# Kernel tuning notes

Measured on AMD Instinct MI355X. Metric: run time of the kernel, lower is better.

The kernel has to match this reference:

```python
import jax, jax.numpy as jnp
import numpy as np


def _lsa_numpy(cost):
    """O(n^3) Jonker-Volgenant / Hungarian (shortest augmenting path with
    potentials). Returns col[i] = column assigned to row i. Matches
    scipy.optimize.linear_sum_assignment for square cost matrices."""
    n = cost.shape[0]
    u = np.zeros(n + 1)
    v = np.zeros(n + 1)
    p = np.zeros(n + 1, dtype=np.int64)   # p[j] = row matched to column j (1-based)
    way = np.zeros(n + 1, dtype=np.int64)
    for i in range(1, n + 1):
        p[0] = i
        j0 = 0
        minv = np.full(n + 1, np.inf)
        used = np.zeros(n + 1, dtype=bool)
        while True:
            used[j0] = True
            i0 = p[j0]
            free = ~used
            free[0] = False
            cur = cost[i0 - 1] - u[i0] - v[1:]
            better = free[1:] & (cur < minv[1:])
            minv[1:] = np.where(better, cur, minv[1:])
            way[1:] = np.where(better, j0, way[1:])
            masked = np.where(free[1:], minv[1:], np.inf)
            j1 = int(np.argmin(masked)) + 1
            delta = masked[j1 - 1]
            u[p[used]] += delta
            v[used] -= delta
            minv[1:] = np.where(free[1:], minv[1:] - delta, minv[1:])
            j0 = j1
            if p[j0] == 0:
                break
        while j0 != 0:
            j1 = int(way[j0])
            p[j0] = p[j1]
            j0 = j1
    col = np.zeros(n, dtype=np.int64)
    for j in range(1, n + 1):
        col[p[j] - 1] = j - 1
    return col


def _batched_lsa(costs):
    costs = np.asarray(costs, dtype=np.float64)
    return np.stack([_lsa_numpy(c) for c in costs]).astype(np.int32)


def _pairwise_dist(pred, target):
    # (B,L,1,D) - (B,1,L,D) -> L2 norm over D, matching torch.norm(x-y, dim=-1)
    return jnp.linalg.norm(pred[:, :, None, :] - target[:, None, :, :], axis=-1)


def setup_inputs() -> dict:
    key = jax.random.key(0)
    k1, k2 = jax.random.split(key)
    B, L, D = 16, 256, 128
    pred = jax.random.normal(k1, (B, L, D), dtype=jnp.float32)
    target = jax.random.normal(k2, (B, L, D), dtype=jnp.float32)
    return {"pred": pred, "target": target}


def reference(pred, target):
    B, L, _ = pred.shape
    dist = _pairwise_dist(pred, target)  # (B, L, L)
    # Hungarian assignment on the detached cost matrices (host callback, like
    # the original's .detach().cpu().numpy() + scipy linear_sum_assignment).
    cols = jax.pure_callback(
        _batched_lsa,
        jax.ShapeDtypeStruct((B, L), jnp.int32),
        jax.lax.stop_gradient(dist),
    )
    # dist[b, r, cols[b, r]] for all rows; reduction='mean' per batch, summed
    # then divided by B == global mean over all matched pairs.
    matched = jnp.take_along_axis(dist, cols[:, :, None], axis=2)[..., 0]  # (B, L)
    return jnp.mean(matched)
```

## Files before the change

### kernel.cpp

```cpp
#include <hip/hip_runtime.h>
#include <hip/hip_fp16.h>
#include <hip/hip_bf16.h>
#include <float.h>
#include <limits.h>

#define B_SZ 16
#define L_SZ 256
#define D_SZ 128

__global__ __launch_bounds__(256) void dist_kernel(const float* __restrict__ pred,
                                                   const float* __restrict__ target,
                                                   float* __restrict__ dist) {
    __shared__ float predRows[8][D_SZ];
    const int blk = blockIdx.x;
    const int b   = blk >> 5;
    const int i0  = (blk & 31) * 8;
    const int tid = threadIdx.x;

    for (int idx = tid; idx < 8 * D_SZ; idx += 256) {
        int r = idx >> 7, d = idx & (D_SZ - 1);
        predRows[r][d] = pred[((size_t)b * L_SZ + i0 + r) * D_SZ + d];
    }
    __syncthreads();

    const int j = tid;
    const float* tr = target + ((size_t)b * L_SZ + j) * D_SZ;
    float acc[8];
#pragma unroll
    for (int r = 0; r < 8; ++r) acc[r] = 0.0f;

    for (int d = 0; d < D_SZ; d += 4) {
        float4 tv = *(const float4*)(tr + d);
#pragma unroll
        for (int r = 0; r < 8; ++r) {
            float4 pv = *(const float4*)(&predRows[r][d]);
            float dx = pv.x - tv.x; acc[r] += dx * dx;
            float dy = pv.y - tv.y; acc[r] += dy * dy;
            float dz = pv.z - tv.z; acc[r] += dz * dz;
            float dw = pv.w - tv.w; acc[r] += dw * dw;
        }
    }
#pragma unroll
    for (int r = 0; r < 8; ++r)
        dist[((size_t)b * L_SZ + i0 + r) * L_SZ + j] = sqrtf(acc[r]);
}

__device__ inline int readlane_i(int x, int l) { return __builtin_amdgcn_readlane(x, l); }
__device__ inline float readlane_f(float x, int l) {
    return __uint_as_float((unsigned)__builtin_amdgcn_readlane((int)__float_as_uint(x), l));
}
__device__ inline unsigned uminu(unsigned a, unsigned b) { return a < b ? a : b; }
template <int CTRL>
__device__ inline unsigned dpp_mov(unsigned v) {
    return (unsigned)__builtin_amdgcn_update_dpp((int)v, (int)v, CTRL, 0xF, 0xF, false);
}
__device__ inline unsigned wave_umin_bcast(unsigned v) {
    unsigned a = dpp_mov<0x111>(v);
    unsigned b = dpp_mov<0x112>(v);
    v = uminu(uminu(v, a), b);
    a = dpp_mov<0x113>(v);
    b = dpp_mov<0x116>(v);
    v = uminu(uminu(v, a), b);
    a = dpp_mov<0x119>(v);
    v = uminu(v, a);
    a = dpp_mov<0x142>(v);
    v = uminu(v, a);
    a = dpp_mov<0x143>(v);
    v = uminu(v, a);
    return (unsigned)__builtin_amdgcn_readlane((int)v, 63);
}
__device__ inline void unpack4(uint2 pk, float& a, float& b, float& c, float& d) {
    union { unsigned u; __half2 h; } x, y; x.u = pk.x; y.u = pk.y;
    a = __low2float(x.h); b = __high2float(x.h);
    c = __low2float(y.h); d = __high2float(y.h);
}
#define SEL4(a0,a1,a2,a3,k) ((k)==0?(a0):(k)==1?(a1):(k)==2?(a2):(a3))

#define OFF_U      (L_SZ * L_SZ * 2)
#define OFF_CLAIM  (OFF_U + (L_SZ + 1) * 4)
#define OFF_FL     (OFF_CLAIM + (L_SZ + 1) * 4)
#define LSA_LDS_BYTES (OFF_FL + (L_SZ + 1) * 4 + 4)

__global__ __launch_bounds__(64) void lsa_kernel(const float* __restrict__ dist,
                                                 double* __restrict__ partial) {
    extern __shared__ char smem[];
    float* u_lds   = (float*)(smem + OFF_U);
    int*   claimed = (int*)(smem + OFF_CLAIM);
    int*   fl      = (int*)(smem + OFF_FL);

    const int b = blockIdx.x;
    const int t = threadIdx.x;
    const float* cost = dist + (size_t)b * L_SZ * L_SZ;
    const int c0i = 4 * t, c1i = 4 * t + 1, c2i = 4 * t + 2, c3i = 4 * t + 3;

    for (int idx = t * 4; idx < L_SZ * L_SZ; idx += 256) {
        float4 f = *(const float4*)(cost + idx);
        union { unsigned u; __half2 h; } a, c;
        a.h = __floats2half2_rn(f.x, f.y);
        c.h = __floats2half2_rn(f.z, f.w);
        uint2 pk; pk.x = a.u; pk.y = c.u;
        *(uint2*)(smem + idx * 2) = pk;
    }
    __syncthreads();

    float bv0 = FLT_MAX, bv1 = FLT_MAX, bv2 = FLT_MAX, bv3 = FLT_MAX;
    int   br0 = 0, br1 = 0, br2 = 0, br3 = 0;
    for (int i = 1; i <= L_SZ; ++i) {
        uint2 cpk = *(const uint2*)(smem + (size_t)(i - 1) * (L_SZ * 2) + t * 8);
        float c0, c1, c2, c3; unpack4(cpk, c0, c1, c2, c3);
        if (c0 < bv0) { bv0 = c0; br0 = i; }
        if (c1 < bv1) { bv1 = c1; br1 = i; }
        if (c2 < bv2) { bv2 = c2; br2 = i; }
        if (c3 < bv3) { bv3 = c3; br3 = i; }
    }
    float v0 = bv0, v1 = bv1, v2 = bv2, v3 = bv3;

    for (int r = t; r <= L_SZ; r += 64) claimed[r] = INT_MAX;
    __syncthreads();
    atomicMin(&claimed[br0], c0i);
    atomicMin(&claimed[br1], c1i);
    atomicMin(&claimed[br2], c2i);
    atomicMin(&claimed[br3], c3i);
    __syncthreads();
    int p0 = (claimed[br0] == c0i) ? br0 : 0;
    int p1 = (claimed[br1] == c1i) ? br1 : 0;
    int p2 = (claimed[br2] == c2i) ? br2 : 0;
    int p3 = (claimed[br3] == c3i) ? br3 : 0;

    int nf = 0;
    for (int blk = 0; blk < 4; ++blk) {
        int r = blk * 64 + t + 1;
        bool isfree = (claimed[r] == INT_MAX);
        unsigned long long mask = __ballot(isfree);
        int before = __popcll(mask & ((1ULL << t) - 1ULL));
        if (isfree) fl[nf + before] = r;
        nf += (int)__popcll(mask);
    }
    __syncthreads();

    int numfree = nf;
    int budget = 1024;
    for (int pass = 0; pass < 2; ++pass) {
        int kq = 0, prv = numfree; numfree = 0;
        while (kq < prv && budget > 0) {
            budget--;
            int i = fl[kq]; kq++;
            uint2 cpk = *(const uint2*)(smem + (size_t)(i - 1) * (L_SZ * 2) + t * 8);
            float cc0, cc1, cc2, cc3; unpack4(cpk, cc0, cc1, cc2, cc3);
            float rc0 = cc0 - v0, rc1 = cc1 - v1, rc2 = cc2 - v2, rc3 = cc3 - v3;
            float m1 = rc0; int j1 = c0i; float m2 = FLT_MAX; int j2 = INT_MAX;
            if (rc1 < m1) { m2 = m1; j2 = j1; m1 = rc1; j1 = c1i; } else if (rc1 < m2) { m2 = rc1; j2 = c1i; }
            if (rc2 < m1) { m2 = m1; j2 = j1; m1 = rc2; j1 = c2i; } else if (rc2 < m2) { m2 = rc2; j2 = c2i; }
            if (rc3 < m1) { m2 = m1; j2 = j1; m1 = rc3; j1 = c3i; } else if (rc3 < m2) { m2 = rc3; j2 = c3i; }
#pragma unroll
            for (int off = 1; off < 64; off <<= 1) {
                float bm1 = __shfl_xor(m1, off, 64); int bj1 = __shfl_xor(j1, off, 64);
                float bm2 = __shfl_xor(m2, off, 64); int bj2 = __shfl_xor(j2, off, 64);
                bool bw = (bm1 < m1) || (bm1 == m1 && bj1 < j1);
                if (bw) {
                    if (bm2 < m1 || (bm2 == m1 && bj2 < j1)) { m2 = bm2; j2 = bj2; }
                    else { m2 = m1; j2 = j1; }
                    m1 = bm1; j1 = bj1;
                } else {
                    if (bm1 < m2 || (bm1 == m2 && bj1 < j2)) { m2 = bm1; j2 = bj1; }
                }
            }
            int t1 = j1 >> 2, k1 = j1 & 3;
            int i0 = readlane_i(SEL4(p0, p1, p2, p3, k1), t1);
            bool strict = (m1 < m2);
            int jt, i0t;
            if (strict) {
                jt = j1; i0t = i0;
                float amt = m2 - m1;
                if (t == t1) {
                    if (k1 == 0) v0 -= amt; else if (k1 == 1) v1 -= amt;
                    else if (k1 == 2) v2 -= amt; else v3 -= amt;
                }
            } else if (i0 != 0) {
                jt = j2; i0t = readlane_i(SEL4(p0, p1, p2, p3, j2 & 3), j2 >> 2);
            } else { jt = j1; i0t = 0; }
            {
                int tt = jt >> 2, kk = jt & 3;
                if (t == tt) {
                    if (kk == 0) p0 = i; else if (kk == 1) p1 = i;
                    else if (kk == 2) p2 = i; else p3 = i;
                }
            }
            if (i0t != 0) {
                if (strict) { kq--; if (t == 0) fl[kq] = i0t; }
                else        { if (t == 0) fl[numfree] = i0t; numfree++; }
            }
            __syncthreads();
        }
        if (budget <= 0) break;
    }

    __syncthreads();
    for (int r = t; r <= L_SZ; r += 64) { claimed[r] = 0; u_lds[r] = 0.0f; }
    __syncthreads();
    if (p0) claimed[p0] = 1;
    if (p1) claimed[p1] = 1;
    if (p2) claimed[p2] = 1;
    if (p3) claimed[p3] = 1;
    __syncthreads();
    int nfree = 0;
    for (int blk = 0; blk < 4; ++blk) {
        int r = blk * 64 + t + 1;
        bool isfree = (claimed[r] == 0);
        unsigned long long mask = __ballot(isfree);
        int before = __popcll(mask & ((1ULL << t) - 1ULL));
        if (isfree) fl[nfree + before] = r;
        nfree += (int)__popcll(mask);
    }
    __syncthreads();
    float pu0 = 0.f, pu1 = 0.f, pu2 = 0.f, pu3 = 0.f;
    const __half* ch = (const __half*)smem;
    if (p0) { pu0 = __half2float(ch[(size_t)(p0 - 1) * L_SZ + c0i]) - v0; u_lds[p0] = pu0; }
    if (p1) { pu1 = __half2float(ch[(size_t)(p1 - 1) * L_SZ + c1i]) - v1; u_lds[p1] = pu1; }
    if (p2) { pu2 = __half2float(ch[(size_t)(p2 - 1) * L_SZ + c2i]) - v2; u_lds[p2] = pu2; }
    if (p3) { pu3 = __half2float(ch[(size_t)(p3 - 1) * L_SZ + c3i]) - v3; u_lds[p3] = pu3; }
    __syncthreads();

    const unsigned HB  = __float_as_uint(1e30f) & 0xFFFFFF00u;
    const unsigned hp0 = HB | (unsigned)c0i, hp1 = HB | (unsigned)c1i;
    const unsigned hp2 = HB | (unsigned)c2i, hp3 = HB | (unsigned)c3i;
    float vsh0 = v0, vsh1 = v1, vsh2 = v2, vsh3 = v3;

    for (int f = 0; f < nfree; ++f) {
        const int icur = fl[f];
        unsigned s0 = 0x7F7FFF00u | (unsigned)c0i;
        unsigned s1 = 0x7F7FFF00u | (unsigned)c1i;
        unsigned s2 = 0x7F7FFF00u | (unsigned)c2i;
        unsigned s3 = 0x7F7FFF00u | (unsigned)c3i;
        int w0 = -1, w1 = -1, w2 = -1, w3 = -1;
        float ds0 = 0.f, ds1 = 0.f, ds2 = 0.f, ds3 = 0.f;
        int   irow = icur;
        float ui0 = u_lds[icur];
        float dj0 = 0.f;
        int   j0  = -1;
        int jS = 0; float dfin = 0.f;

        for (int it = 0; it <= L_SZ; ++it) {
            uint2 cpk = *(const uint2*)(smem + (size_t)(irow - 1) * (L_SZ * 2) + t * 8);
            float cc0, cc1, cc2, cc3; unpack4(cpk, cc0, cc1, cc2, cc3);
            const float base = dj0 - ui0;
            float n0 = fmaxf((cc0 - vsh0) + base, 0.0f);
            float n1 = fmaxf((cc1 - vsh1) + base, 0.0f);
            float n2 = fmaxf((cc2 - vsh2) + base, 0.0f);
            float n3 = fmaxf((cc3 - vsh3) + base, 0.0f);
            unsigned np0 = (__float_as_uint(n0) & 0xFFFFFF00u) | (unsigned)c0i;
            unsigned np1 = (__float_as_uint(n1) & 0xFFFFFF00u) | (unsigned)c1i;
            unsigned np2 = (__float_as_uint(n2) & 0xFFFFFF00u) | (unsigned)c2i;
            unsigned np3 = (__float_as_uint(n3) & 0xFFFFFF00u) | (unsigned)c3i;
            bool b0 = np0 < s0, b1 = np1 < s1, b2 = np2 < s2, b3 = np3 < s3;
            w0 = b0 ? j0 : w0;  s0 = b0 ? np0 : s0;
            w1 = b1 ? j0 : w1;  s1 = b1 ? np1 : s1;
            w2 = b2 ? j0 : w2;  s2 = b2 ? np2 : s2;
            w3 = b3 ? j0 : w3;  s3 = b3 ? np3 : s3;

            unsigned m01 = uminu(s0, s1), m23 = uminu(s2, s3);
            unsigned m4  = uminu(m01, m23);
            int kloc = (int)(m4 & 3u);
            int   myi = SEL4(p0, p1, p2, p3, kloc);
            float myu = SEL4(pu0, pu1, pu2, pu3, kloc);

            const unsigned pk = wave_umin_bcast(m4);
            const int   j1    = (int)(pk & 255u);
            const int   t1    = j1 >> 2;
            const float delta = __uint_as_float(pk & 0xFFFFFF00u);
            const int   i1    = readlane_i(myi, t1);
            const float u1    = readlane_f(myu, t1);

            if (i1 == 0 || it == L_SZ) { jS = j1; dfin = delta; break; }

            bool e0 = (c0i == j1), e1 = (c1i == j1), e2 = (c2i == j1), e3 = (c3i == j1);
            vsh0 = e0 ? -1e30f : vsh0;  s0 = e0 ? hp0 : s0;  ds0 = e0 ? delta : ds0;
            vsh1 = e1 ? -1e30f : vsh1;  s1 = e1 ? hp1 : s1;  ds1 = e1 ? delta : ds1;
            vsh2 = e2 ? -1e30f : vsh2;  s2 = e2 ? hp2 : s2;  ds2 = e2 ? delta : ds2;
            vsh3 = e3 ? -1e30f : vsh3;  s3 = e3 ? hp3 : s3;  ds3 = e3 ? delta : ds3;

            j0 = j1; dj0 = delta; ui0 = u1; irow = i1;
        }

        if (vsh0 < -1e29f) { u_lds[p0] += dfin - ds0; v0 += ds0 - dfin; }
        if (vsh1 < -1e29f) { u_lds[p1] += dfin - ds1; v1 += ds1 - dfin; }
        if (vsh2 < -1e29f) { u_lds[p2] += dfin - ds2; v2 += ds2 - dfin; }
        if (vsh3 < -1e29f) { u_lds[p3] += dfin - ds3; v3 += ds3 - dfin; }
        if (t == 0) u_lds[icur] += dfin;
        vsh0 = v0; vsh1 = v1; vsh2 = v2; vsh3 = v3;
        __syncthreads();

        int j = jS;
        for (int st = 0; st <= L_SZ; ++st) {
            int tj = j >> 2, kj = j & 3;
            int jn = readlane_i(SEL4(w0, w1, w2, w3, kj), tj);
            int pn;
            if (jn < 0) pn = icur;
            else pn = readlane_i(SEL4(p0, p1, p2, p3, jn & 3), jn >> 2);
            if (t == tj) {
                if (kj == 0) p0 = pn; else if (kj == 1) p1 = pn;
                else if (kj == 2) p2 = pn; else p3 = pn;
            }
            if (jn < 0) break;
            j = jn;
        }
        __syncthreads();
        pu0 = u_lds[p0]; pu1 = u_lds[p1]; pu2 = u_lds[p2]; pu3 = u_lds[p3];
        __syncthreads();
    }

    double s = 0.0;
    s += (double)cost[(size_t)max(p0 - 1, 0) * L_SZ + c0i];
    s += (double)cost[(size_t)max(p1 - 1, 0) * L_SZ + c1i];
    s += (double)cost[(size_t)max(p2 - 1, 0) * L_SZ + c2i];
    s += (double)cost[(size_t)max(p3 - 1, 0) * L_SZ + c3i];
#pragma unroll
    for (int off = 1; off < 64; off <<= 1) s += __shfl_xor(s, off, 64);
    if (t == 0) partial[b] = s;
}

__global__ void finalize_kernel(const double* __restrict__ partial, float* __restrict__ out) {
    double s = 0.0;
    for (int b = 0; b < B_SZ; ++b) s += partial[b];
    out[0] = (float)(s / (double)(B_SZ * L_SZ));
}

extern "C" void kernel_launch(void* const* d_in, const int* in_sizes, int n_in,
                              void* d_out, int out_size, void* d_ws, size_t ws_size,
                              hipStream_t stream) {
    const float* pred   = (const float*)d_in[0];
    const float* target = (const float*)d_in[1];
    float* out = (float*)d_out;

    float*  dist    = (float*)d_ws;
    double* partial = (double*)((char*)d_ws + (size_t)B_SZ * L_SZ * L_SZ * sizeof(float));

    (void)hipFuncSetAttribute((const void*)lsa_kernel,
                              hipFuncAttributeMaxDynamicSharedMemorySize,
                              LSA_LDS_BYTES);

    dist_kernel<<<B_SZ * L_SZ / 8, 256, 0, stream>>>(pred, target, dist);
    lsa_kernel<<<B_SZ, 64, LSA_LDS_BYTES, stream>>>(dist, partial);
    finalize_kernel<<<1, 1, 0, stream>>>(partial, out);
}
```

Before: 2.170 ms.

## Speculatively prefetch next Dijkstra row using second-smallest slack candidate

In the Hungarian shortest-augmenting-path inner loop, each lane now keeps both its minimum and second-minimum packed slack. A second wave-wide min reduction predicts the next column to be selected, and that row's cost data is loaded from LDS ahead of time. When the prediction matches the actual next column, the dependent LDS load drops off the serial critical path. The cost is an extra DPP reduction, readlane and LDS load on every iteration, and the prediction can be stale because newly scanned rows lower slacks.

Measured after the change: 2.382 ms. 1.1x slower.

```diff
diff --git a/kernel.cpp b/kernel.cpp
--- a/kernel.cpp
+++ b/kernel.cpp
@@ -50,6 +50,7 @@
     return __uint_as_float((unsigned)__builtin_amdgcn_readlane((int)__float_as_uint(x), l));
 }
 __device__ inline unsigned uminu(unsigned a, unsigned b) { return a < b ? a : b; }
+__device__ inline unsigned umaxu(unsigned a, unsigned b) { return a < b ? b : a; }
 template <int CTRL>
 __device__ inline unsigned dpp_mov(unsigned v) {
     return (unsigned)__builtin_amdgcn_update_dpp((int)v, (int)v, CTRL, 0xF, 0xF, false);
@@ -234,15 +235,17 @@
         unsigned s3 = 0x7F7FFF00u | (unsigned)c3i;
         int w0 = -1, w1 = -1, w2 = -1, w3 = -1;
         float ds0 = 0.f, ds1 = 0.f, ds2 = 0.f, ds3 = 0.f;
-        int   irow = icur;
         float ui0 = u_lds[icur];
         float dj0 = 0.f;
         int   j0  = -1;
         int jS = 0; float dfin = 0.f;
 
+        uint2 cur = *(const uint2*)(smem + (size_t)(icur - 1) * (L_SZ * 2) + t * 8);
+        int specJ = -1; bool specValid = false;
+        uint2 specData; specData.x = 0; specData.y = 0;
+
         for (int it = 0; it <= L_SZ; ++it) {
-            uint2 cpk = *(const uint2*)(smem + (size_t)(irow - 1) * (L_SZ * 2) + t * 8);
-            float cc0, cc1, cc2, cc3; unpack4(cpk, cc0, cc1, cc2, cc3);
+            float cc0, cc1, cc2, cc3; unpack4(cur, cc0, cc1, cc2, cc3);
             const float base = dj0 - ui0;
             float n0 = fmaxf((cc0 - vsh0) + base, 0.0f);
             float n1 = fmaxf((cc1 - vsh1) + base, 0.0f);
@@ -258,16 +261,18 @@
             w2 = b2 ? j0 : w2;  s2 = b2 ? np2 : s2;
             w3 = b3 ? j0 : w3;  s3 = b3 ? np3 : s3;
 
-            unsigned m01 = uminu(s0, s1), m23 = uminu(s2, s3);
-            unsigned m4  = uminu(m01, m23);
-            int kloc = (int)(m4 & 3u);
+            unsigned m01 = uminu(s0, s1), M01 = umaxu(s0, s1);
+            unsigned m23 = uminu(s2, s3), M23 = umaxu(s2, s3);
+            unsigned a   = uminu(m01, m23);
+            unsigned bb  = uminu(umaxu(m01, m23), uminu(M01, M23));
+            int kloc = (int)(a & 3u);
             int   myi = SEL4(p0, p1, p2, p3, kloc);
             float myu = SEL4(pu0, pu1, pu2, pu3, kloc);
 
-            const unsigned pk = wave_umin_bcast(m4);
-            const int   j1    = (int)(pk & 255u);
+            const unsigned o1 = wave_umin_bcast(a);
+            const int   j1    = (int)(o1 & 255u);
             const int   t1    = j1 >> 2;
-            const float delta = __uint_as_float(pk & 0xFFFFFF00u);
+            const float delta = __uint_as_float(o1 & 0xFFFFFF00u);
             const int   i1    = readlane_i(myi, t1);
             const float u1    = readlane_f(myu, t1);
 
@@ -279,7 +284,21 @@
             vsh2 = e2 ? -1e30f : vsh2;  s2 = e2 ? hp2 : s2;  ds2 = e2 ? delta : ds2;
             vsh3 = e3 ? -1e30f : vsh3;  s3 = e3 ? hp3 : s3;  ds3 = e3 ? delta : ds3;
 
-            j0 = j1; dj0 = delta; ui0 = u1; irow = i1;
+            if (specValid && j1 == specJ) {
+                cur = specData;
+            } else {
+                cur = *(const uint2*)(smem + (size_t)(i1 - 1) * (L_SZ * 2) + t * 8);
+            }
+
+            unsigned a2 = (a == o1) ? bb : a;
+            const unsigned o2 = wave_umin_bcast(a2);
+            const int j2 = (int)(o2 & 255u);
+            const int i2 = readlane_i(SEL4(p0, p1, p2, p3, j2 & 3), j2 >> 2);
+            specJ = j2; specValid = (i2 != 0);
+            if (specValid)
+                specData = *(const uint2*)(smem + (size_t)(i2 - 1) * (L_SZ * 2) + t * 8);
+
+            j0 = j1; dj0 = delta; ui0 = u1;
         }
 
         if (vsh0 < -1e29f) { u_lds[p0] += dfin - ds0; v0 += ds0 - dfin; }
```
